# Optimization experiments

Measured on AMD Instinct MI355X. Metric: run time of the kernel, lower is better.

The kernel has to match this reference:

```python
import jax, jax.numpy as jnp
import numpy as np

N = 10000
E = 320000
D_IN = 256
D_OUT = 256
EPS = 0.2  # initial value of trainable eps


def setup_inputs() -> dict:
    key = jax.random.key(0)
    ks = jax.random.split(key, 7)
    x = jax.random.normal(ks[0], (N, D_IN), dtype=jnp.float32)
    edge_index = jax.random.randint(ks[1], (2, E), 0, N, dtype=jnp.int64)
    # MLP params (Linear(in,out) -> ReLU -> Linear(out,out)), Kaiming-ish scale
    w1 = jax.random.normal(ks[2], (D_IN, D_OUT), dtype=jnp.float32) / np.sqrt(D_IN)
    b1 = jnp.zeros((D_OUT,), dtype=jnp.float32)
    w2 = jax.random.normal(ks[3], (D_OUT, D_OUT), dtype=jnp.float32) / np.sqrt(D_OUT)
    b2 = jnp.zeros((D_OUT,), dtype=jnp.float32)
    eps = jnp.float32(EPS)
    return {"x": x, "edge_index": edge_index, "w1": w1, "b1": b1,
            "w2": w2, "b2": b2, "eps": eps}


def reference(x, edge_index, w1, b1, w2, b2, eps):
    src, dst = edge_index[0], edge_index[1]
    # GIN sum aggregation: agg[i] = sum_{(j->i) in E} x[j]
    msgs = x[src]  # [E, D_IN] gather
    agg = jax.ops.segment_sum(msgs, dst, num_segments=N)  # [N, D_IN] scatter-add
    h = (1.0 + eps) * x + agg
    # 2-layer MLP
    h = jax.nn.relu(h @ w1 + b1)
    out = h @ w2 + b2
    return out
```

## Files before the change

### kernel.cpp

```cpp
#include <hip/hip_runtime.h>

#define NN 10000
#define NE 320000
#define CAP 96

typedef __bf16 bf16x8 __attribute__((ext_vector_type(8)));
typedef float f32x4 __attribute__((ext_vector_type(4)));

static __device__ __forceinline__ unsigned short f2bf(float f) {
  union { float fv; unsigned u; } v; v.fv = f;
  unsigned r = v.u + 0x7FFFu + ((v.u >> 16) & 1u);
  return (unsigned short)(r >> 16);
}
static __device__ __forceinline__ float bf2f(unsigned short b) {
  union { unsigned u; float f; } v; v.u = ((unsigned)b) << 16;
  return v.f;
}


__global__ __launch_bounds__(256) void conv_k(const float* __restrict__ x,
                                              const float* __restrict__ w1,
                                              const float* __restrict__ w2,
                                              ushort4* __restrict__ xb4,
                                              unsigned short* __restrict__ w1t,
                                              unsigned short* __restrict__ w2t,
                                              int* __restrict__ cnt) {
  int t = blockIdx.x * 256 + threadIdx.x;
  if (t < 10240) cnt[t] = 0;
  if (t < 640000) {
    float4 v = reinterpret_cast<const float4*>(x)[t];
    ushort4 o;
    o.x = f2bf(v.x); o.y = f2bf(v.y); o.z = f2bf(v.z); o.w = f2bf(v.w);
    xb4[t] = o;
  } else {
    int u = t - 640000;
    if (u < 65536) {
      int n = u >> 8, k = u & 255;
      w1t[u] = f2bf(w1[k * 256 + n]);
    } else if (u < 131072) {
      int q = u - 65536;
      int n = q >> 8, k = q & 255;
      w2t[q] = f2bf(w2[k * 256 + n]);
    }
  }
}


__global__ __launch_bounds__(256) void fill_k(const int* __restrict__ ei,
                                              int* __restrict__ cnt,
                                              int* __restrict__ bucket) {
  int e2 = blockIdx.x * 256 + threadIdx.x;
  int e = e2 * 2;
  if (e < NE) {
    int2 s = *reinterpret_cast<const int2*>(&ei[e]);
    int2 d = *reinterpret_cast<const int2*>(&ei[NE + e]);
    int p0 = atomicAdd(&cnt[d.x], 1);
    if (p0 < CAP) bucket[d.x * CAP + p0] = s.x;
    int p1 = atomicAdd(&cnt[d.y], 1);
    if (p1 < CAP) bucket[d.y * CAP + p1] = s.y;
  }
}


__global__ __launch_bounds__(256) void agg_k(const ushort4* __restrict__ xb4,
                                             const int* __restrict__ cnt,
                                             const int* __restrict__ bucket,
                                             const float* __restrict__ epsp,
                                             unsigned short* __restrict__ hb) {
  int node = blockIdx.x * 4 + (threadIdx.x >> 6);
  if (node >= NN) return;
  int lane = threadIdx.x & 63;
  ushort4 s = xb4[node * 64 + lane];
  float e1 = 1.0f + epsp[0];
  float a0 = bf2f(s.x) * e1, a1 = bf2f(s.y) * e1;
  float a2 = bf2f(s.z) * e1, a3 = bf2f(s.w) * e1;
  int n = min(cnt[node], CAP);
  const int* bp = bucket + node * CAP;
  int k = 0;
  for (; k + 3 < n; k += 4) {
    int i0 = bp[k], i1 = bp[k + 1], i2 = bp[k + 2], i3 = bp[k + 3];
    ushort4 v0 = xb4[i0 * 64 + lane];
    ushort4 v1 = xb4[i1 * 64 + lane];
    ushort4 v2 = xb4[i2 * 64 + lane];
    ushort4 v3 = xb4[i3 * 64 + lane];
    a0 += (bf2f(v0.x) + bf2f(v1.x)) + (bf2f(v2.x) + bf2f(v3.x));
    a1 += (bf2f(v0.y) + bf2f(v1.y)) + (bf2f(v2.y) + bf2f(v3.y));
    a2 += (bf2f(v0.z) + bf2f(v1.z)) + (bf2f(v2.z) + bf2f(v3.z));
    a3 += (bf2f(v0.w) + bf2f(v1.w)) + (bf2f(v2.w) + bf2f(v3.w));
  }
  for (; k < n; ++k) {
    ushort4 v0 = xb4[bp[k] * 64 + lane];
    a0 += bf2f(v0.x); a1 += bf2f(v0.y); a2 += bf2f(v0.z); a3 += bf2f(v0.w);
  }
  ushort4 o;
  o.x = f2bf(a0); o.y = f2bf(a1); o.z = f2bf(a2); o.w = f2bf(a3);
  reinterpret_cast<ushort4*>(hb)[node * 64 + lane] = o;
}


__global__ __launch_bounds__(256) void mlp_k(const unsigned short* __restrict__ hb,
                                             const unsigned short* __restrict__ w1t,
                                             const float* __restrict__ b1,
                                             const unsigned short* __restrict__ w2t,
                                             const float* __restrict__ b2,
                                             float* __restrict__ out) {
  __shared__ unsigned short As[32][264];
  __shared__ unsigned short Bs[256][72];
  int m0 = blockIdx.x * 32;
  int tid = threadIdx.x;
  int lane = tid & 63, wave = tid >> 6;
  int waveM = wave & 1, waveN = wave >> 1;
  int l15 = lane & 15, g = lane >> 4;

#pragma unroll
  for (int i = 0; i < 4; ++i) {
    int c = tid + i * 256;
    int r = c >> 5, cc = c & 31;
    int4 v = (m0 + r < NN)
                 ? *reinterpret_cast<const int4*>(&hb[(m0 + r) * 256 + cc * 8])
                 : make_int4(0, 0, 0, 0);
    *reinterpret_cast<int4*>(&As[r][cc * 8]) = v;
  }

  float bias1[8], bias2[8];
#pragma unroll
  for (int ni = 0; ni < 8; ++ni) {
    int col = waveN * 128 + ni * 16 + l15;
    bias1[ni] = b1[col];
    bias2[ni] = b2[col];
  }

  f32x4 acc[8];
#pragma unroll
  for (int ni = 0; ni < 8; ++ni) acc[ni] = f32x4{0.f, 0.f, 0.f, 0.f};

  for (int k0 = 0; k0 < 256; k0 += 64) {
#pragma unroll
    for (int i = 0; i < 8; ++i) {
      int c = tid + i * 256;
      int n = c >> 3, kc = c & 7;
      *reinterpret_cast<int4*>(&Bs[n][kc * 8]) =
          *reinterpret_cast<const int4*>(&w1t[n * 256 + k0 + kc * 8]);
    }
    __syncthreads();
#pragma unroll
    for (int kk = 0; kk < 2; ++kk) {
      bf16x8 af = *reinterpret_cast<const bf16x8*>(
          &As[waveM * 16 + l15][k0 + kk * 32 + g * 8]);
#pragma unroll
      for (int ni = 0; ni < 8; ++ni) {
        bf16x8 bfr = *reinterpret_cast<const bf16x8*>(
            &Bs[waveN * 128 + ni * 16 + l15][kk * 32 + g * 8]);
        acc[ni] = __builtin_amdgcn_mfma_f32_16x16x32_bf16(af, bfr, acc[ni], 0, 0, 0);
      }
    }
    __syncthreads();
  }

#pragma unroll
  for (int ni = 0; ni < 8; ++ni) {
    int col = waveN * 128 + ni * 16 + l15;
#pragma unroll
    for (int r = 0; r < 4; ++r) {
      int row = waveM * 16 + g * 4 + r;
      As[row][col] = f2bf(fmaxf(acc[ni][r] + bias1[ni], 0.f));
    }
    acc[ni] = f32x4{0.f, 0.f, 0.f, 0.f};
  }

  for (int k0 = 0; k0 < 256; k0 += 64) {
#pragma unroll
    for (int i = 0; i < 8; ++i) {
      int c = tid + i * 256;
      int n = c >> 3, kc = c & 7;
      *reinterpret_cast<int4*>(&Bs[n][kc * 8]) =
          *reinterpret_cast<const int4*>(&w2t[n * 256 + k0 + kc * 8]);
    }
    __syncthreads();
#pragma unroll
    for (int kk = 0; kk < 2; ++kk) {
      bf16x8 af = *reinterpret_cast<const bf16x8*>(
          &As[waveM * 16 + l15][k0 + kk * 32 + g * 8]);
#pragma unroll
      for (int ni = 0; ni < 8; ++ni) {
        bf16x8 bfr = *reinterpret_cast<const bf16x8*>(
            &Bs[waveN * 128 + ni * 16 + l15][kk * 32 + g * 8]);
        acc[ni] = __builtin_amdgcn_mfma_f32_16x16x32_bf16(af, bfr, acc[ni], 0, 0, 0);
      }
    }
    __syncthreads();
  }

#pragma unroll
  for (int ni = 0; ni < 8; ++ni) {
    int col = waveN * 128 + ni * 16 + l15;
#pragma unroll
    for (int r = 0; r < 4; ++r) {
      int row = m0 + waveM * 16 + g * 4 + r;
      if (row < NN) out[row * 256 + col] = acc[ni][r] + bias2[ni];
    }
  }
}


extern "C" void kernel_launch(void* const* d_in, const int* in_sizes, int n_in,
                              void* d_out, int out_size, void* d_ws, size_t ws_size,
                              hipStream_t stream) {
  const float* x = (const float*)d_in[0];
  const int* ei = (const int*)d_in[1];
  const float* w1 = (const float*)d_in[2];
  const float* b1 = (const float*)d_in[3];
  const float* w2 = (const float*)d_in[4];
  const float* b2 = (const float*)d_in[5];
  const float* eps = (const float*)d_in[6];
  float* out = (float*)d_out;

  int* cnt = (int*)d_ws;
  int* bucket = cnt + 10240;
  unsigned short* xb = (unsigned short*)(bucket + NN * CAP);
  unsigned short* w1t = xb + NN * 256;
  unsigned short* w2t = w1t + 65536;
  unsigned short* hb = w2t + 65536;

  conv_k<<<(640000 + 131072) / 256, 256, 0, stream>>>(
      x, w1, w2, (ushort4*)xb, w1t, w2t, cnt);
  fill_k<<<(NE / 2 + 255) / 256, 256, 0, stream>>>(ei, cnt, bucket);
  agg_k<<<(NN + 3) / 4, 256, 0, stream>>>((const ushort4*)xb, cnt, bucket, eps, hb);
  mlp_k<<<(NN + 31) / 32, 256, 0, stream>>>(hb, w1t, b1, w2t, b2, out);
}
```

Before: 68.65 us.

## Fuse neighbor aggregation into MLP kernel and tile weight transpose via LDS

The gather-sum aggregation is moved into the MLP kernel, so each block aggregates its own 32 rows directly into shared memory. This drops the hb intermediate round trip and one kernel launch. The weight transpose now goes through shared-memory 64x64 tiles with coalesced float4 reads and 16-byte writes, and the edge fill handles four edges per thread. The MLP B-tile is halved to a K-step of 32, which uses less LDS but needs more syncs. Only 313 blocks run the aggregation, so the latency-bound gather now has far less parallelism than the previous 2500 blocks.

```diff
diff --git a/kernel.cpp b/kernel.cpp
--- a/kernel.cpp
+++ b/kernel.cpp
@@ -6,6 +6,7 @@
 
 typedef __bf16 bf16x8 __attribute__((ext_vector_type(8)));
 typedef float f32x4 __attribute__((ext_vector_type(4)));
+typedef unsigned short us8 __attribute__((ext_vector_type(8)));
 
 static __device__ __forceinline__ unsigned short f2bf(float f) {
   union { float fv; unsigned u; } v; v.fv = f;
@@ -25,22 +26,37 @@
                                               unsigned short* __restrict__ w1t,
                                               unsigned short* __restrict__ w2t,
                                               int* __restrict__ cnt) {
-  int t = blockIdx.x * 256 + threadIdx.x;
-  if (t < 10240) cnt[t] = 0;
-  if (t < 640000) {
+  __shared__ unsigned short sh[64][72];
+  int bid = blockIdx.x, tid = threadIdx.x;
+  if (bid < 2500) {
+    int t = bid * 256 + tid;
+    if (t < 10240) cnt[t] = 0;
     float4 v = reinterpret_cast<const float4*>(x)[t];
     ushort4 o;
     o.x = f2bf(v.x); o.y = f2bf(v.y); o.z = f2bf(v.z); o.w = f2bf(v.w);
     xb4[t] = o;
   } else {
-    int u = t - 640000;
-    if (u < 65536) {
-      int n = u >> 8, k = u & 255;
-      w1t[u] = f2bf(w1[k * 256 + n]);
-    } else if (u < 131072) {
-      int q = u - 65536;
-      int n = q >> 8, k = q & 255;
-      w2t[q] = f2bf(w2[k * 256 + n]);
+    int b2 = bid - 2500;
+    const float* w = (b2 & 16) ? w2 : w1;
+    unsigned short* wt = (b2 & 16) ? w2t : w1t;
+    int tile = b2 & 15;
+    int ki0 = (tile >> 2) * 64, ni0 = (tile & 3) * 64;
+    int r = tid >> 4, c = tid & 15;
+#pragma unroll
+    for (int rr = r; rr < 64; rr += 16) {
+      float4 v = *reinterpret_cast<const float4*>(&w[(ki0 + rr) * 256 + ni0 + c * 4]);
+      ushort4 o;
+      o.x = f2bf(v.x); o.y = f2bf(v.y); o.z = f2bf(v.z); o.w = f2bf(v.w);
+      *reinterpret_cast<ushort4*>(&sh[rr][c * 4]) = o;
+    }
+    __syncthreads();
+    int n = tid >> 3, c8 = tid & 7;
+#pragma unroll
+    for (int nn = n; nn < 64; nn += 32) {
+      us8 o;
+#pragma unroll
+      for (int j = 0; j < 8; ++j) o[j] = sh[c8 * 8 + j][nn];
+      *reinterpret_cast<us8*>(&wt[(ni0 + nn) * 256 + ki0 + c8 * 8]) = o;
     }
   }
 }
@@ -49,77 +65,66 @@
 __global__ __launch_bounds__(256) void fill_k(const int* __restrict__ ei,
                                               int* __restrict__ cnt,
                                               int* __restrict__ bucket) {
-  int e2 = blockIdx.x * 256 + threadIdx.x;
-  int e = e2 * 2;
+  int e = (blockIdx.x * 256 + threadIdx.x) * 4;
   if (e < NE) {
-    int2 s = *reinterpret_cast<const int2*>(&ei[e]);
-    int2 d = *reinterpret_cast<const int2*>(&ei[NE + e]);
-    int p0 = atomicAdd(&cnt[d.x], 1);
-    if (p0 < CAP) bucket[d.x * CAP + p0] = s.x;
-    int p1 = atomicAdd(&cnt[d.y], 1);
-    if (p1 < CAP) bucket[d.y * CAP + p1] = s.y;
-  }
-}
-
-
-__global__ __launch_bounds__(256) void agg_k(const ushort4* __restrict__ xb4,
-                                             const int* __restrict__ cnt,
-                                             const int* __restrict__ bucket,
-                                             const float* __restrict__ epsp,
-                                             unsigned short* __restrict__ hb) {
-  int node = blockIdx.x * 4 + (threadIdx.x >> 6);
-  if (node >= NN) return;
-  int lane = threadIdx.x & 63;
-  ushort4 s = xb4[node * 64 + lane];
-  float e1 = 1.0f + epsp[0];
-  float a0 = bf2f(s.x) * e1, a1 = bf2f(s.y) * e1;
-  float a2 = bf2f(s.z) * e1, a3 = bf2f(s.w) * e1;
-  int n = min(cnt[node], CAP);
-  const int* bp = bucket + node * CAP;
-  int k = 0;
-  for (; k + 3 < n; k += 4) {
-    int i0 = bp[k], i1 = bp[k + 1], i2 = bp[k + 2], i3 = bp[k + 3];
-    ushort4 v0 = xb4[i0 * 64 + lane];
-    ushort4 v1 = xb4[i1 * 64 + lane];
-    ushort4 v2 = xb4[i2 * 64 + lane];
-    ushort4 v3 = xb4[i3 * 64 + lane];
-    a0 += (bf2f(v0.x) + bf2f(v1.x)) + (bf2f(v2.x) + bf2f(v3.x));
-    a1 += (bf2f(v0.y) + bf2f(v1.y)) + (bf2f(v2.y) + bf2f(v3.y));
-    a2 += (bf2f(v0.z) + bf2f(v1.z)) + (bf2f(v2.z) + bf2f(v3.z));
-    a3 += (bf2f(v0.w) + bf2f(v1.w)) + (bf2f(v2.w) + bf2f(v3.w));
-  }
-  for (; k < n; ++k) {
-    ushort4 v0 = xb4[bp[k] * 64 + lane];
-    a0 += bf2f(v0.x); a1 += bf2f(v0.y); a2 += bf2f(v0.z); a3 += bf2f(v0.w);
-  }
-  ushort4 o;
-  o.x = f2bf(a0); o.y = f2bf(a1); o.z = f2bf(a2); o.w = f2bf(a3);
-  reinterpret_cast<ushort4*>(hb)[node * 64 + lane] = o;
-}
-
-
-__global__ __launch_bounds__(256) void mlp_k(const unsigned short* __restrict__ hb,
-                                             const unsigned short* __restrict__ w1t,
-                                             const float* __restrict__ b1,
-                                             const unsigned short* __restrict__ w2t,
-                                             const float* __restrict__ b2,
-                                             float* __restrict__ out) {
+    int4 s = *reinterpret_cast<const int4*>(&ei[e]);
+    int4 d = *reinterpret_cast<const int4*>(&ei[NE + e]);
+    int p;
+    p = atomicAdd(&cnt[d.x], 1); if (p < CAP) bucket[d.x * CAP + p] = s.x;
+    p = atomicAdd(&cnt[d.y], 1); if (p < CAP) bucket[d.y * CAP + p] = s.y;
+    p = atomicAdd(&cnt[d.z], 1); if (p < CAP) bucket[d.z * CAP + p] = s.z;
+    p = atomicAdd(&cnt[d.w], 1); if (p < CAP) bucket[d.w * CAP + p] = s.w;
+  }
+}
+
+
+__global__ __launch_bounds__(256) void fused_k(const ushort4* __restrict__ xb4,
+                                               const int* __restrict__ cnt,
+                                               const int* __restrict__ bucket,
+                                               const float* __restrict__ epsp,
+                                               const unsigned short* __restrict__ w1t,
+                                               const float* __restrict__ b1,
+                                               const unsigned short* __restrict__ w2t,
+                                               const float* __restrict__ b2,
+                                               float* __restrict__ out) {
   __shared__ unsigned short As[32][264];
-  __shared__ unsigned short Bs[256][72];
+  __shared__ unsigned short Bs[256][40];
   int m0 = blockIdx.x * 32;
-  int tid = threadIdx.x;
-  int lane = tid & 63, wave = tid >> 6;
+  int tid = threadIdx.x, lane = tid & 63, wave = tid >> 6;
   int waveM = wave & 1, waveN = wave >> 1;
   int l15 = lane & 15, g = lane >> 4;
-
-#pragma unroll
-  for (int i = 0; i < 4; ++i) {
-    int c = tid + i * 256;
-    int r = c >> 5, cc = c & 31;
-    int4 v = (m0 + r < NN)
-                 ? *reinterpret_cast<const int4*>(&hb[(m0 + r) * 256 + cc * 8])
-                 : make_int4(0, 0, 0, 0);
-    *reinterpret_cast<int4*>(&As[r][cc * 8]) = v;
+  float e1 = 1.0f + epsp[0];
+
+  for (int i = 0; i < 8; ++i) {
+    int row = wave * 8 + i;
+    int node = m0 + row;
+    float a0 = 0.f, a1 = 0.f, a2 = 0.f, a3 = 0.f;
+    if (node < NN) {
+      ushort4 s = xb4[node * 64 + lane];
+      a0 = bf2f(s.x) * e1; a1 = bf2f(s.y) * e1;
+      a2 = bf2f(s.z) * e1; a3 = bf2f(s.w) * e1;
+      int n = min(cnt[node], CAP);
+      const int* bp = bucket + node * CAP;
+      int k = 0;
+      for (; k + 3 < n; k += 4) {
+        int i0 = bp[k], i1 = bp[k + 1], i2 = bp[k + 2], i3 = bp[k + 3];
+        ushort4 v0 = xb4[i0 * 64 + lane];
+        ushort4 v1 = xb4[i1 * 64 + lane];
+        ushort4 v2 = xb4[i2 * 64 + lane];
+        ushort4 v3 = xb4[i3 * 64 + lane];
+        a0 += (bf2f(v0.x) + bf2f(v1.x)) + (bf2f(v2.x) + bf2f(v3.x));
+        a1 += (bf2f(v0.y) + bf2f(v1.y)) + (bf2f(v2.y) + bf2f(v3.y));
+        a2 += (bf2f(v0.z) + bf2f(v1.z)) + (bf2f(v2.z) + bf2f(v3.z));
+        a3 += (bf2f(v0.w) + bf2f(v1.w)) + (bf2f(v2.w) + bf2f(v3.w));
+      }
+      for (; k < n; ++k) {
+        ushort4 v0 = xb4[bp[k] * 64 + lane];
+        a0 += bf2f(v0.x); a1 += bf2f(v0.y); a2 += bf2f(v0.z); a3 += bf2f(v0.w);
+      }
+    }
+    ushort4 o;
+    o.x = f2bf(a0); o.y = f2bf(a1); o.z = f2bf(a2); o.w = f2bf(a3);
+    *reinterpret_cast<ushort4*>(&As[row][lane * 4]) = o;
   }
 
   float bias1[8], bias2[8];
@@ -134,25 +139,21 @@
 #pragma unroll
   for (int ni = 0; ni < 8; ++ni) acc[ni] = f32x4{0.f, 0.f, 0.f, 0.f};
 
-  for (int k0 = 0; k0 < 256; k0 += 64) {
-#pragma unroll
-    for (int i = 0; i < 8; ++i) {
-      int c = tid + i * 256;
-      int n = c >> 3, kc = c & 7;
+  for (int k0 = 0; k0 < 256; k0 += 32) {
+#pragma unroll
+    for (int i = 0; i < 4; ++i) {
+      int idx = tid + i * 256;
+      int n = idx >> 2, kc = idx & 3;
       *reinterpret_cast<int4*>(&Bs[n][kc * 8]) =
           *reinterpret_cast<const int4*>(&w1t[n * 256 + k0 + kc * 8]);
     }
     __syncthreads();
-#pragma unroll
-    for (int kk = 0; kk < 2; ++kk) {
-      bf16x8 af = *reinterpret_cast<const bf16x8*>(
-          &As[waveM * 16 + l15][k0 + kk * 32 + g * 8]);
-#pragma unroll
-      for (int ni = 0; ni < 8; ++ni) {
-        bf16x8 bfr = *reinterpret_cast<const bf16x8*>(
-            &Bs[waveN * 128 + ni * 16 + l15][kk * 32 + g * 8]);
-        acc[ni] = __builtin_amdgcn_mfma_f32_16x16x32_bf16(af, bfr, acc[ni], 0, 0, 0);
-      }
+    bf16x8 af = *reinterpret_cast<const bf16x8*>(&As[waveM * 16 + l15][k0 + g * 8]);
+#pragma unroll
+    for (int ni = 0; ni < 8; ++ni) {
+      bf16x8 bfr = *reinterpret_cast<const bf16x8*>(
+          &Bs[waveN * 128 + ni * 16 + l15][g * 8]);
+      acc[ni] = __builtin_amdgcn_mfma_f32_16x16x32_bf16(af, bfr, acc[ni], 0, 0, 0);
     }
     __syncthreads();
   }
@@ -168,25 +169,21 @@
     acc[ni] = f32x4{0.f, 0.f, 0.f, 0.f};
   }
 
-  for (int k0 = 0; k0 < 256; k0 += 64) {
-#pragma unroll
-    for (int i = 0; i < 8; ++i) {
-      int c = tid + i * 256;
-      int n = c >> 3, kc = c & 7;
+  for (int k0 = 0; k0 < 256; k0 += 32) {
+#pragma unroll
+    for (int i = 0; i < 4; ++i) {
+      int idx = tid + i * 256;
+      int n = idx >> 2, kc = idx & 3;
       *reinterpret_cast<int4*>(&Bs[n][kc * 8]) =
           *reinterpret_cast<const int4*>(&w2t[n * 256 + k0 + kc * 8]);
     }
     __syncthreads();
-#pragma unroll
-    for (int kk = 0; kk < 2; ++kk) {
-      bf16x8 af = *reinterpret_cast<const bf16x8*>(
-          &As[waveM * 16 + l15][k0 + kk * 32 + g * 8]);
-#pragma unroll
-      for (int ni = 0; ni < 8; ++ni) {
-        bf16x8 bfr = *reinterpret_cast<const bf16x8*>(
-            &Bs[waveN * 128 + ni * 16 + l15][kk * 32 + g * 8]);
-        acc[ni] = __builtin_amdgcn_mfma_f32_16x16x32_bf16(af, bfr, acc[ni], 0, 0, 0);
-      }
+    bf16x8 af = *reinterpret_cast<const bf16x8*>(&As[waveM * 16 + l15][k0 + g * 8]);
+#pragma unroll
+    for (int ni = 0; ni < 8; ++ni) {
+      bf16x8 bfr = *reinterpret_cast<const bf16x8*>(
+          &Bs[waveN * 128 + ni * 16 + l15][g * 8]);
+      acc[ni] = __builtin_amdgcn_mfma_f32_16x16x32_bf16(af, bfr, acc[ni], 0, 0, 0);
     }
     __syncthreads();
   }
@@ -220,11 +217,9 @@
   unsigned short* xb = (unsigned short*)(bucket + NN * CAP);
   unsigned short* w1t = xb + NN * 256;
   unsigned short* w2t = w1t + 65536;
-  unsigned short* hb = w2t + 65536;
-
-  conv_k<<<(640000 + 131072) / 256, 256, 0, stream>>>(
-      x, w1, w2, (ushort4*)xb, w1t, w2t, cnt);
-  fill_k<<<(NE / 2 + 255) / 256, 256, 0, stream>>>(ei, cnt, bucket);
-  agg_k<<<(NN + 3) / 4, 256, 0, stream>>>((const ushort4*)xb, cnt, bucket, eps, hb);
-  mlp_k<<<(NN + 31) / 32, 256, 0, stream>>>(hb, w1t, b1, w2t, b2, out);
-}
+
+  conv_k<<<2532, 256, 0, stream>>>(x, w1, w2, (ushort4*)xb, w1t, w2t, cnt);
+  fill_k<<<(NE / 4 + 255) / 256, 256, 0, stream>>>(ei, cnt, bucket);
+  fused_k<<<(NN + 31) / 32, 256, 0, stream>>>((const ushort4*)xb, cnt, bucket, eps,
+                                              w1t, b1, w2t, b2, out);
+}
```

Result: slower. 105.2 us (+53.2%).

## Fuse all stages into one cooperative persistent kernel with grid syncs

Applied to the files above, without the earlier changes.

Replaces the four separate launches (convert, bucket fill, aggregate, MLP) with a single cooperative kernel of 512 blocks of 512 threads that uses grid.sync between phases. This removes launch gaps and inter-kernel drain. It also transposes the weights through a shared-memory tile, fills buckets four edges per thread, and splits each node's gather across two half-waves using 16-byte loads. The four-kernel path stays as a fallback if the cooperative launch fails. Grid-wide barriers and the smaller per-block MLP tiles (k step of 32) may cost some throughput in the compute phases.

```diff
diff --git a/kernel.cpp b/kernel.cpp
--- a/kernel.cpp
+++ b/kernel.cpp
@@ -1,11 +1,19 @@
 #include <hip/hip_runtime.h>
+#include <hip/hip_cooperative_groups.h>
+
+namespace cg = cooperative_groups;
 
 #define NN 10000
 #define NE 320000
 #define CAP 96
+#define CBLK 512
+#define CTHR 512
+#define CTOT (CBLK * CTHR)
+#define CWAVES (CBLK * 8)
 
 typedef __bf16 bf16x8 __attribute__((ext_vector_type(8)));
 typedef float f32x4 __attribute__((ext_vector_type(4)));
+typedef unsigned short us8 __attribute__((ext_vector_type(8)));
 
 static __device__ __forceinline__ unsigned short f2bf(float f) {
   union { float fv; unsigned u; } v; v.fv = f;
@@ -15,6 +23,210 @@
 static __device__ __forceinline__ float bf2f(unsigned short b) {
   union { unsigned u; float f; } v; v.u = ((unsigned)b) << 16;
   return v.f;
+}
+
+
+__global__ __launch_bounds__(CTHR, 4) void mega2_k(
+    const float* __restrict__ x, const int* __restrict__ ei,
+    const float* __restrict__ w1, const float* __restrict__ b1,
+    const float* __restrict__ w2, const float* __restrict__ b2,
+    const float* __restrict__ epsp, float* __restrict__ out,
+    int* __restrict__ cnt, int* __restrict__ bucket,
+    unsigned short* __restrict__ xb, unsigned short* __restrict__ w1t,
+    unsigned short* __restrict__ w2t, unsigned short* __restrict__ hb) {
+  __shared__ unsigned short AsM[32][264];
+  __shared__ unsigned short Bs[256][40];
+  cg::grid_group grid = cg::this_grid();
+  const int tid = threadIdx.x;
+  const int bid = blockIdx.x;
+  const int gtid = bid * CTHR + tid;
+
+  if (gtid < 10240) cnt[gtid] = 0;
+  for (int t = gtid; t < 640000; t += CTOT) {
+    float4 v = reinterpret_cast<const float4*>(x)[t];
+    ushort4 o;
+    o.x = f2bf(v.x); o.y = f2bf(v.y); o.z = f2bf(v.z); o.w = f2bf(v.w);
+    reinterpret_cast<ushort4*>(xb)[t] = o;
+  }
+  grid.sync();
+
+  if (gtid < NE / 4) {
+    int e = gtid * 4;
+    int4 s = *reinterpret_cast<const int4*>(&ei[e]);
+    int4 d = *reinterpret_cast<const int4*>(&ei[NE + e]);
+    int p;
+    p = atomicAdd(&cnt[d.x], 1); if (p < CAP) bucket[d.x * CAP + p] = s.x;
+    p = atomicAdd(&cnt[d.y], 1); if (p < CAP) bucket[d.y * CAP + p] = s.y;
+    p = atomicAdd(&cnt[d.z], 1); if (p < CAP) bucket[d.z * CAP + p] = s.z;
+    p = atomicAdd(&cnt[d.w], 1); if (p < CAP) bucket[d.w * CAP + p] = s.w;
+  }
+  if (bid >= CBLK - 32) {
+    unsigned short* sh = &AsM[0][0];
+    int b2 = bid - (CBLK - 32);
+    const float* w = (b2 & 16) ? w2 : w1;
+    unsigned short* wt = (b2 & 16) ? w2t : w1t;
+    int tile = b2 & 15;
+    int ki0 = (tile >> 2) * 64, ni0 = (tile & 3) * 64;
+    if (tid < 256) {
+      int r = tid >> 4, c = tid & 15;
+#pragma unroll
+      for (int rr = r; rr < 64; rr += 16) {
+        float4 v = *reinterpret_cast<const float4*>(&w[(ki0 + rr) * 256 + ni0 + c * 4]);
+        ushort4 o;
+        o.x = f2bf(v.x); o.y = f2bf(v.y); o.z = f2bf(v.z); o.w = f2bf(v.w);
+        *reinterpret_cast<ushort4*>(&sh[rr * 72 + c * 4]) = o;
+      }
+    }
+    __syncthreads();
+    if (tid < 256) {
+      int nidx = tid >> 3, c8 = tid & 7;
+#pragma unroll
+      for (int nn2 = nidx; nn2 < 64; nn2 += 32) {
+        us8 o;
+#pragma unroll
+        for (int j = 0; j < 8; ++j) o[j] = sh[(c8 * 8 + j) * 72 + nn2];
+        *reinterpret_cast<us8*>(&wt[(ni0 + nn2) * 256 + ki0 + c8 * 8]) = o;
+      }
+    }
+  }
+  grid.sync();
+
+  {
+    const us8* xb8 = (const us8*)xb;
+    int wv = (bid << 3) + (tid >> 6);
+    int lane = tid & 63;
+    int half = lane >> 5, off = lane & 31;
+    float e1 = 1.0f + epsp[0];
+    float selfw = half ? 0.0f : e1;
+    for (int node = wv; node < NN; node += CWAVES) {
+      us8 sv = xb8[node * 32 + off];
+      float a[8];
+#pragma unroll
+      for (int j = 0; j < 8; ++j) a[j] = bf2f(sv[j]) * selfw;
+      int n = min(cnt[node], CAP);
+      const int4* bp4 = (const int4*)(bucket + node * CAP);
+      int4 ia = bp4[0], ib = bp4[1];
+      int k = 0;
+      while (k + 8 <= n) {
+        int4 na = bp4[(k >> 2) + 2];
+        int4 nb = bp4[(k >> 2) + 3];
+        int r0 = half ? ia.y : ia.x;
+        int r1 = half ? ia.w : ia.z;
+        int r2 = half ? ib.y : ib.x;
+        int r3 = half ? ib.w : ib.z;
+        us8 v0 = xb8[r0 * 32 + off];
+        us8 v1 = xb8[r1 * 32 + off];
+        us8 v2 = xb8[r2 * 32 + off];
+        us8 v3 = xb8[r3 * 32 + off];
+#pragma unroll
+        for (int j = 0; j < 8; ++j)
+          a[j] += (bf2f(v0[j]) + bf2f(v1[j])) + (bf2f(v2[j]) + bf2f(v3[j]));
+        ia = na; ib = nb; k += 8;
+      }
+      int tl = n - k;
+#pragma unroll
+      for (int p = 0; p < 4; ++p) {
+        int idx = (p == 0) ? (half ? ia.y : ia.x)
+                : (p == 1) ? (half ? ia.w : ia.z)
+                : (p == 2) ? (half ? ib.y : ib.x)
+                           : (half ? ib.w : ib.z);
+        if (2 * p + half < tl) {
+          us8 v = xb8[idx * 32 + off];
+#pragma unroll
+          for (int j = 0; j < 8; ++j) a[j] += bf2f(v[j]);
+        }
+      }
+#pragma unroll
+      for (int j = 0; j < 8; ++j) a[j] += __shfl_xor(a[j], 32);
+      if (half == 0) {
+        us8 o;
+#pragma unroll
+        for (int j = 0; j < 8; ++j) o[j] = f2bf(a[j]);
+        *reinterpret_cast<us8*>(&hb[node * 256 + off * 8]) = o;
+      }
+    }
+  }
+  grid.sync();
+
+  if (bid < (NN + 31) / 32) {
+    int m0 = bid * 32;
+    int lane = tid & 63, wave = tid >> 6;
+    int waveM = wave & 1, waveN = wave >> 1;
+    int l15 = lane & 15, g = lane >> 4;
+#pragma unroll
+    for (int i = 0; i < 2; ++i) {
+      int idx = tid + i * CTHR;
+      int r = idx >> 5, c8 = idx & 31;
+      int row = m0 + r;
+      int4 v = (row < NN) ? *reinterpret_cast<const int4*>(&hb[row * 256 + c8 * 8])
+                          : make_int4(0, 0, 0, 0);
+      *reinterpret_cast<int4*>(&AsM[r][c8 * 8]) = v;
+    }
+    float bias1[4], bias2[4];
+#pragma unroll
+    for (int ni = 0; ni < 4; ++ni) {
+      int col = waveN * 64 + ni * 16 + l15;
+      bias1[ni] = b1[col];
+      bias2[ni] = b2[col];
+    }
+    f32x4 acc[4];
+#pragma unroll
+    for (int ni = 0; ni < 4; ++ni) acc[ni] = f32x4{0.f, 0.f, 0.f, 0.f};
+
+    for (int k0 = 0; k0 < 256; k0 += 32) {
+#pragma unroll
+      for (int i = 0; i < 2; ++i) {
+        int idx = tid + i * CTHR;
+        int nrow = idx >> 2, kc = idx & 3;
+        *reinterpret_cast<int4*>(&Bs[nrow][kc * 8]) =
+            *reinterpret_cast<const int4*>(&w1t[nrow * 256 + k0 + kc * 8]);
+      }
+      __syncthreads();
+      bf16x8 af = *reinterpret_cast<const bf16x8*>(&AsM[waveM * 16 + l15][k0 + g * 8]);
+#pragma unroll
+      for (int ni = 0; ni < 4; ++ni) {
+        bf16x8 bfr = *reinterpret_cast<const bf16x8*>(
+            &Bs[waveN * 64 + ni * 16 + l15][g * 8]);
+        acc[ni] = __builtin_amdgcn_mfma_f32_16x16x32_bf16(af, bfr, acc[ni], 0, 0, 0);
+      }
+      __syncthreads();
+    }
+#pragma unroll
+    for (int ni = 0; ni < 4; ++ni) {
+      int col = waveN * 64 + ni * 16 + l15;
+#pragma unroll
+      for (int r = 0; r < 4; ++r)
+        AsM[waveM * 16 + g * 4 + r][col] = f2bf(fmaxf(acc[ni][r] + bias1[ni], 0.f));
+      acc[ni] = f32x4{0.f, 0.f, 0.f, 0.f};
+    }
+    for (int k0 = 0; k0 < 256; k0 += 32) {
+#pragma unroll
+      for (int i = 0; i < 2; ++i) {
+        int idx = tid + i * CTHR;
+        int nrow = idx >> 2, kc = idx & 3;
+        *reinterpret_cast<int4*>(&Bs[nrow][kc * 8]) =
+            *reinterpret_cast<const int4*>(&w2t[nrow * 256 + k0 + kc * 8]);
+      }
+      __syncthreads();
+      bf16x8 af = *reinterpret_cast<const bf16x8*>(&AsM[waveM * 16 + l15][k0 + g * 8]);
+#pragma unroll
+      for (int ni = 0; ni < 4; ++ni) {
+        bf16x8 bfr = *reinterpret_cast<const bf16x8*>(
+            &Bs[waveN * 64 + ni * 16 + l15][g * 8]);
+        acc[ni] = __builtin_amdgcn_mfma_f32_16x16x32_bf16(af, bfr, acc[ni], 0, 0, 0);
+      }
+      __syncthreads();
+    }
+#pragma unroll
+    for (int ni = 0; ni < 4; ++ni) {
+      int col = waveN * 64 + ni * 16 + l15;
+#pragma unroll
+      for (int r = 0; r < 4; ++r) {
+        int row = m0 + waveM * 16 + g * 4 + r;
+        if (row < NN) out[row * 256 + col] = acc[ni][r] + bias2[ni];
+      }
+    }
+  }
 }
 
 
@@ -25,42 +237,55 @@
                                               unsigned short* __restrict__ w1t,
                                               unsigned short* __restrict__ w2t,
                                               int* __restrict__ cnt) {
-  int t = blockIdx.x * 256 + threadIdx.x;
-  if (t < 10240) cnt[t] = 0;
-  if (t < 640000) {
+  __shared__ unsigned short sh[64][72];
+  int bid = blockIdx.x, tid = threadIdx.x;
+  if (bid < 2500) {
+    int t = bid * 256 + tid;
+    if (t < 10240) cnt[t] = 0;
     float4 v = reinterpret_cast<const float4*>(x)[t];
     ushort4 o;
     o.x = f2bf(v.x); o.y = f2bf(v.y); o.z = f2bf(v.z); o.w = f2bf(v.w);
     xb4[t] = o;
   } else {
-    int u = t - 640000;
-    if (u < 65536) {
-      int n = u >> 8, k = u & 255;
-      w1t[u] = f2bf(w1[k * 256 + n]);
-    } else if (u < 131072) {
-      int q = u - 65536;
-      int n = q >> 8, k = q & 255;
-      w2t[q] = f2bf(w2[k * 256 + n]);
-    }
-  }
-}
-
+    int b2 = bid - 2500;
+    const float* w = (b2 & 16) ? w2 : w1;
+    unsigned short* wt = (b2 & 16) ? w2t : w1t;
+    int tile = b2 & 15;
+    int ki0 = (tile >> 2) * 64, ni0 = (tile & 3) * 64;
+    int r = tid >> 4, c = tid & 15;
+#pragma unroll
+    for (int rr = r; rr < 64; rr += 16) {
+      float4 v = *reinterpret_cast<const float4*>(&w[(ki0 + rr) * 256 + ni0 + c * 4]);
+      ushort4 o;
+      o.x = f2bf(v.x); o.y = f2bf(v.y); o.z = f2bf(v.z); o.w = f2bf(v.w);
+      *reinterpret_cast<ushort4*>(&sh[rr][c * 4]) = o;
+    }
+    __syncthreads();
+    int n = tid >> 3, c8 = tid & 7;
+#pragma unroll
+    for (int nn = n; nn < 64; nn += 32) {
+      us8 o;
+#pragma unroll
+      for (int j = 0; j < 8; ++j) o[j] = sh[c8 * 8 + j][nn];
+      *reinterpret_cast<us8*>(&wt[(ni0 + nn) * 256 + ki0 + c8 * 8]) = o;
+    }
+  }
+}
 
 __global__ __launch_bounds__(256) void fill_k(const int* __restrict__ ei,
                                               int* __restrict__ cnt,
                                               int* __restrict__ bucket) {
-  int e2 = blockIdx.x * 256 + threadIdx.x;
-  int e = e2 * 2;
+  int e = (blockIdx.x * 256 + threadIdx.x) * 4;
   if (e < NE) {
-    int2 s = *reinterpret_cast<const int2*>(&ei[e]);
-    int2 d = *reinterpret_cast<const int2*>(&ei[NE + e]);
-    int p0 = atomicAdd(&cnt[d.x], 1);
-    if (p0 < CAP) bucket[d.x * CAP + p0] = s.x;
-    int p1 = atomicAdd(&cnt[d.y], 1);
-    if (p1 < CAP) bucket[d.y * CAP + p1] = s.y;
-  }
-}
-
+    int4 s = *reinterpret_cast<const int4*>(&ei[e]);
+    int4 d = *reinterpret_cast<const int4*>(&ei[NE + e]);
+    int p;
+    p = atomicAdd(&cnt[d.x], 1); if (p < CAP) bucket[d.x * CAP + p] = s.x;
+    p = atomicAdd(&cnt[d.y], 1); if (p < CAP) bucket[d.y * CAP + p] = s.y;
+    p = atomicAdd(&cnt[d.z], 1); if (p < CAP) bucket[d.z * CAP + p] = s.z;
+    p = atomicAdd(&cnt[d.w], 1); if (p < CAP) bucket[d.w * CAP + p] = s.w;
+  }
+}
 
 __global__ __launch_bounds__(256) void agg_k(const ushort4* __restrict__ xb4,
                                              const int* __restrict__ cnt,
@@ -97,7 +322,6 @@
   reinterpret_cast<ushort4*>(hb)[node * 64 + lane] = o;
 }
 
-
 __global__ __launch_bounds__(256) void mlp_k(const unsigned short* __restrict__ hb,
                                              const unsigned short* __restrict__ w1t,
                                              const float* __restrict__ b1,
@@ -111,7 +335,6 @@
   int lane = tid & 63, wave = tid >> 6;
   int waveM = wave & 1, waveN = wave >> 1;
   int l15 = lane & 15, g = lane >> 4;
-
 #pragma unroll
   for (int i = 0; i < 4; ++i) {
     int c = tid + i * 256;
@@ -121,7 +344,6 @@
                  : make_int4(0, 0, 0, 0);
     *reinterpret_cast<int4*>(&As[r][cc * 8]) = v;
   }
-
   float bias1[8], bias2[8];
 #pragma unroll
   for (int ni = 0; ni < 8; ++ni) {
@@ -129,11 +351,9 @@
     bias1[ni] = b1[col];
     bias2[ni] = b2[col];
   }
-
   f32x4 acc[8];
 #pragma unroll
   for (int ni = 0; ni < 8; ++ni) acc[ni] = f32x4{0.f, 0.f, 0.f, 0.f};
-
   for (int k0 = 0; k0 < 256; k0 += 64) {
 #pragma unroll
     for (int i = 0; i < 8; ++i) {
@@ -156,7 +376,6 @@
     }
     __syncthreads();
   }
-
 #pragma unroll
   for (int ni = 0; ni < 8; ++ni) {
     int col = waveN * 128 + ni * 16 + l15;
@@ -167,7 +386,6 @@
     }
     acc[ni] = f32x4{0.f, 0.f, 0.f, 0.f};
   }
-
   for (int k0 = 0; k0 < 256; k0 += 64) {
 #pragma unroll
     for (int i = 0; i < 8; ++i) {
@@ -190,7 +408,6 @@
     }
     __syncthreads();
   }
-
 #pragma unroll
   for (int ni = 0; ni < 8; ++ni) {
     int col = waveN * 128 + ni * 16 + l15;
@@ -217,14 +434,21 @@
 
   int* cnt = (int*)d_ws;
   int* bucket = cnt + 10240;
-  unsigned short* xb = (unsigned short*)(bucket + NN * CAP);
+  unsigned short* xb = (unsigned short*)(bucket + NN * CAP + 16);
   unsigned short* w1t = xb + NN * 256;
   unsigned short* w2t = w1t + 65536;
   unsigned short* hb = w2t + 65536;
 
-  conv_k<<<(640000 + 131072) / 256, 256, 0, stream>>>(
-      x, w1, w2, (ushort4*)xb, w1t, w2t, cnt);
-  fill_k<<<(NE / 2 + 255) / 256, 256, 0, stream>>>(ei, cnt, bucket);
-  agg_k<<<(NN + 3) / 4, 256, 0, stream>>>((const ushort4*)xb, cnt, bucket, eps, hb);
-  mlp_k<<<(NN + 31) / 32, 256, 0, stream>>>(hb, w1t, b1, w2t, b2, out);
-}
+  void* kargs[] = {(void*)&x,   (void*)&ei,     (void*)&w1,  (void*)&b1,
+                   (void*)&w2,  (void*)&b2,     (void*)&eps, (void*)&out,
+                   (void*)&cnt, (void*)&bucket, (void*)&xb,  (void*)&w1t,
+                   (void*)&w2t, (void*)&hb};
+  hipError_t err = hipLaunchCooperativeKernel((void*)mega2_k, dim3(CBLK),
+                                              dim3(CTHR), kargs, 0, stream);
+  if (err != hipSuccess) {
+    conv_k<<<2532, 256, 0, stream>>>(x, w1, w2, (ushort4*)xb, w1t, w2t, cnt);
+    fill_k<<<(NE / 4 + 255) / 256, 256, 0, stream>>>(ei, cnt, bucket);
+    agg_k<<<(NN + 3) / 4, 256, 0, stream>>>((const ushort4*)xb, cnt, bucket, eps, hb);
+    mlp_k<<<(NN + 31) / 32, 256, 0, stream>>>(hb, w1t, b1, w2t, b2, out);
+  }
+}
```

Measured after the change: 238.4 us. 247% more time.
